# Performance work log

Measured on AMD Instinct MI355X. Metric: run time of the kernel, lower is better.

Reference implementation:

```python
import jax, jax.numpy as jnp
import numpy as np


def _rot_mat(thetas, scales):
    # thetas, scales: [bs, g] -> [bs, g, 9, 9] bilinear-interpolation matrices
    bs, g = thetas.shape
    t = thetas.reshape(-1)
    s = scales.reshape(-1)
    x = jnp.cos(t) * s
    y = jnp.sin(t) * s
    yp = -y
    z = jnp.zeros_like(x)
    o = jnp.ones_like(x)
    a = x - y; b = x * y; c = x + y; d = a * c; e = a + c
    ap = x - yp; bp = x * yp; cp = x + yp; dp = ap * cp; ep = ap + cp

    def M(rows):
        # rows: 9 lists of 9 [N]-arrays -> [9, 9, N]
        return jnp.stack([jnp.stack(r, axis=0) for r in rows], axis=0)

    ctr = [z, z, z, z, o, z, z, z, z]

    pb1 = M([
        [a, 1 - a, z, z, z, z, z, z, z],
        [z, 1 - y, y, z, z, z, z, z, z],
        [z, z, a, z, z, 1 - a, z, z, z],
        [y, z, z, 1 - y, z, z, z, z, z],
        ctr,
        [z, z, z, z, z, 1 - y, z, z, y],
        [z, z, z, 1 - a, z, z, a, z, z],
        [z, z, z, z, z, z, y, 1 - y, z],
        [z, z, z, z, z, z, z, 1 - a, a]])
    pb2 = M([
        [a, 1 - a, z, z, z, z, z, z, z],
        [z, x - b, b, z, 1 - c + b, y - b, z, z, z],
        [z, z, a, z, z, 1 - a, z, z, z],
        [b, y - b, z, x - b, 1 - c + b, z, z, z, z],
        ctr,
        [z, z, z, z, 1 - c + b, x - b, z, y - b, b],
        [z, z, z, 1 - a, z, z, a, z, z],
        [z, z, z, y - b, 1 - c + b, z, b, x - b, z],
        [z, z, z, z, z, z, z, 1 - a, a]])
    ps1 = M([
        [d, a - d, z, c - d, 1 - e + d, z, z, z, z],
        [z, x - b, b, z, 1 - c + b, y - b, z, z, z],
        [z, c - d, d, z, 1 - e + d, a - d, z, z, z],
        [b, y - b, z, x - b, 1 - c + b, z, z, z, z],
        ctr,
        [z, z, z, z, 1 - c + b, x - b, z, y - b, b],
        [z, z, z, a - d, 1 - e + d, z, d, c - d, z],
        [z, z, z, y - b, 1 - c + b, z, b, x - b, z],
        [z, z, z, z, 1 - e + d, c - d, z, a - d, d]])
    ps2 = pb2  # identical in the source
    nb1 = M([
        [cp, z, z, 1 - cp, z, z, z, z, z],
        [yp, 1 - yp, z, z, z, z, z, z, z],
        [z, 1 - cp, cp, z, z, z, z, z, z],
        [z, z, z, 1 - yp, z, z, yp, z, z],
        ctr,
        [z, z, yp, z, z, 1 - yp, z, z, z],
        [z, z, z, z, z, z, cp, 1 - cp, z],
        [z, z, z, z, z, z, z, 1 - yp, yp],
        [z, z, z, z, z, 1 - cp, z, z, cp]])
    nb2 = M([
        [cp, z, z, 1 - cp, z, z, z, z, z],
        [bp, x - bp, z, yp - bp, 1 - cp + bp, z, z, z, z],
        [z, 1 - cp, cp, z, z, z, z, z, z],
        [z, z, z, x - bp, 1 - cp + bp, z, bp, yp - bp, z],
        ctr,
        [z, yp - bp, bp, z, 1 - cp + bp, x - bp, z, z, z],
        [z, z, z, z, z, z, cp, 1 - cp, z],
        [z, z, z, z, 1 - cp + bp, yp - bp, z, x - bp, bp],
        [z, z, z, z, z, 1 - cp, z, z, cp]])
    ns1 = M([
        [dp, cp - dp, z, ap - dp, 1 - ep + dp, z, z, z, z],
        [bp, x - bp, z, yp - bp, 1 - cp + bp, z, z, z, z],
        [z, ap - dp, dp, z, 1 - ep + dp, cp - dp, z, z, z],
        [z, yp - bp, bp, z, 1 - cp + bp, x - bp, z, z, z],
        ctr,
        [z, z, z, x - bp, 1 - cp + bp, z, bp, yp - bp, z],
        [z, z, z, cp - dp, 1 - ep + dp, z, dp, ap - dp, z],
        [z, z, z, z, 1 - cp + bp, yp - bp, z, x - bp, bp],
        [z, z, z, z, 1 - ep + dp, ap - dp, z, cp - dp, dp]])
    ns2 = nb2  # mirrors the positive branch where small_2 == big_2

    m_pos = (t >= 0.0)[None, None, :]
    m_big = (s >= 1.0)[None, None, :]
    m_1 = (jnp.abs(t) <= jnp.pi / 4)[None, None, :]
    pos = jnp.where(m_big, jnp.where(m_1, pb1, pb2), jnp.where(m_1, ps1, ps2))
    neg = jnp.where(m_big, jnp.where(m_1, nb1, nb2), jnp.where(m_1, ns1, ns2))
    rot = jnp.where(m_pos, pos, neg)  # [9, 9, bs*g]
    return jnp.transpose(rot, (2, 0, 1)).reshape(bs, g, 9, 9)


def _forward(x, thetas, scales, lambdas, weight):
    # x: [B, Cin, H, W]; weight: [n, Cout, Cin, 3, 3]; thetas/scales/lambdas: [B, n]
    B, Cin, H, W = x.shape
    n, Cout = weight.shape[0], weight.shape[1]
    rot = _rot_mat(thetas, scales) * lambdas[:, :, None, None]  # [B, n, 9, 9]
    w9 = weight.reshape(n, Cout, Cin, 9)
    # per-sample transformed kernel: sum over kernel_number n and source taps j
    w = jnp.einsum('bnij,nocj->bioc', rot, w9)  # [B, 9, Cout, Cin]
    w = jnp.transpose(w, (0, 2, 3, 1)).reshape(B * Cout, Cin, 3, 3)
    xg = x.reshape(1, B * Cin, H, W)
    out = jax.lax.conv_general_dilated(
        xg, w, window_strides=(1, 1), padding=((1, 1), (1, 1)),
        dimension_numbers=('NCHW', 'OIHW', 'NCHW'), feature_group_count=B)
    return out.reshape(B, Cout, H, W)


def setup_inputs() -> dict:
    key = jax.random.key(0)
    ks = jax.random.split(key, 5)
    B, Cin, Cout, H, W, n = 16, 256, 256, 64, 64, 4
    x = jax.random.normal(ks[0], (B, Cin, H, W), dtype=jnp.float32)
    thetas = jax.random.uniform(ks[1], (B, n), minval=-1.2, maxval=1.2, dtype=jnp.float32)
    scales = jax.random.uniform(ks[2], (B, n), minval=0.5, maxval=1.5, dtype=jnp.float32)
    lambdas = jax.nn.softmax(jax.random.normal(ks[3], (B, n), dtype=jnp.float32), axis=-1)
    weight = jax.random.normal(ks[4], (n, Cout, Cin, 3, 3), dtype=jnp.float32) * 0.05
    return {"x": x, "thetas": thetas, "scales": scales, "lambdas": lambdas, "weight": weight}


def reference(x, thetas, scales, lambdas, weight):
    return _forward(x, thetas, scales, lambdas, weight)
```

## Files before the change

kernel.cpp:

```cpp
#include <hip/hip_runtime.h>
#include <cstdint>
#include <cstddef>

typedef unsigned short ushort_t;
typedef __attribute__((ext_vector_type(4))) float f32x4;
typedef __attribute__((ext_vector_type(8))) short s16x8;

#define PI_4F 0.78539816339744830962f

__device__ inline ushort_t f2bf(float f) {
  unsigned int u = __float_as_uint(f);
  u = u + 0x7fffu + ((u >> 16) & 1u);
  return (ushort_t)(u >> 16);
}

__global__ void rot_kernel(const float* __restrict__ thetas, const float* __restrict__ scales,
                           const float* __restrict__ lambdas, float* __restrict__ rot) {
  int tid = threadIdx.x;
  float t = thetas[tid], s = scales[tid], lam = lambdas[tid];
  float xv = cosf(t) * s, yv = sinf(t) * s;
  bool pos = (t >= 0.0f), big = (s >= 1.0f), m1 = (fabsf(t) <= PI_4F);
  float M[81];
#pragma unroll
  for (int i = 0; i < 81; ++i) M[i] = 0.0f;
  M[36 + 4] = 1.0f;
  if (pos) {
    float a = xv - yv, bb = xv * yv, c = xv + yv;
    if (m1 && big) {
      M[0] = a; M[1] = 1 - a;
      M[9 + 1] = 1 - yv; M[9 + 2] = yv;
      M[18 + 2] = a; M[18 + 5] = 1 - a;
      M[27 + 0] = yv; M[27 + 3] = 1 - yv;
      M[45 + 5] = 1 - yv; M[45 + 8] = yv;
      M[54 + 3] = 1 - a; M[54 + 6] = a;
      M[63 + 6] = yv; M[63 + 7] = 1 - yv;
      M[72 + 7] = 1 - a; M[72 + 8] = a;
    } else if (m1) {
      float d = a * c, e = a + c;
      M[0] = d; M[1] = a - d; M[3] = c - d; M[4] = 1 - e + d;
      M[9 + 1] = xv - bb; M[9 + 2] = bb; M[9 + 4] = 1 - c + bb; M[9 + 5] = yv - bb;
      M[18 + 1] = c - d; M[18 + 2] = d; M[18 + 4] = 1 - e + d; M[18 + 5] = a - d;
      M[27 + 0] = bb; M[27 + 1] = yv - bb; M[27 + 3] = xv - bb; M[27 + 4] = 1 - c + bb;
      M[45 + 4] = 1 - c + bb; M[45 + 5] = xv - bb; M[45 + 7] = yv - bb; M[45 + 8] = bb;
      M[54 + 3] = a - d; M[54 + 4] = 1 - e + d; M[54 + 6] = d; M[54 + 7] = c - d;
      M[63 + 3] = yv - bb; M[63 + 4] = 1 - c + bb; M[63 + 6] = bb; M[63 + 7] = xv - bb;
      M[72 + 4] = 1 - e + d; M[72 + 5] = c - d; M[72 + 7] = a - d; M[72 + 8] = d;
    } else {
      M[0] = a; M[1] = 1 - a;
      M[9 + 1] = xv - bb; M[9 + 2] = bb; M[9 + 4] = 1 - c + bb; M[9 + 5] = yv - bb;
      M[18 + 2] = a; M[18 + 5] = 1 - a;
      M[27 + 0] = bb; M[27 + 1] = yv - bb; M[27 + 3] = xv - bb; M[27 + 4] = 1 - c + bb;
      M[45 + 4] = 1 - c + bb; M[45 + 5] = xv - bb; M[45 + 7] = yv - bb; M[45 + 8] = bb;
      M[54 + 3] = 1 - a; M[54 + 6] = a;
      M[63 + 3] = yv - bb; M[63 + 4] = 1 - c + bb; M[63 + 6] = bb; M[63 + 7] = xv - bb;
      M[72 + 7] = 1 - a; M[72 + 8] = a;
    }
  } else {
    float yp = -yv;
    float ap = xv - yp, bp = xv * yp, cp = xv + yp;
    if (m1 && big) {
      M[0] = cp; M[3] = 1 - cp;
      M[9 + 0] = yp; M[9 + 1] = 1 - yp;
      M[18 + 1] = 1 - cp; M[18 + 2] = cp;
      M[27 + 3] = 1 - yp; M[27 + 6] = yp;
      M[45 + 2] = yp; M[45 + 5] = 1 - yp;
      M[54 + 6] = cp; M[54 + 7] = 1 - cp;
      M[63 + 7] = 1 - yp; M[63 + 8] = yp;
      M[72 + 5] = 1 - cp; M[72 + 8] = cp;
    } else if (m1) {
      float dp = ap * cp, ep = ap + cp;
      M[0] = dp; M[1] = cp - dp; M[3] = ap - dp; M[4] = 1 - ep + dp;
      M[9 + 0] = bp; M[9 + 1] = xv - bp; M[9 + 3] = yp - bp; M[9 + 4] = 1 - cp + bp;
      M[18 + 1] = ap - dp; M[18 + 2] = dp; M[18 + 4] = 1 - ep + dp; M[18 + 5] = cp - dp;
      M[27 + 1] = yp - bp; M[27 + 2] = bp; M[27 + 4] = 1 - cp + bp; M[27 + 5] = xv - bp;
      M[45 + 3] = xv - bp; M[45 + 4] = 1 - cp + bp; M[45 + 6] = bp; M[45 + 7] = yp - bp;
      M[54 + 3] = cp - dp; M[54 + 4] = 1 - ep + dp; M[54 + 6] = dp; M[54 + 7] = ap - dp;
      M[63 + 4] = 1 - cp + bp; M[63 + 5] = yp - bp; M[63 + 7] = xv - bp; M[63 + 8] = bp;
      M[72 + 4] = 1 - ep + dp; M[72 + 5] = ap - dp; M[72 + 7] = cp - dp; M[72 + 8] = dp;
    } else {
      M[0] = cp; M[3] = 1 - cp;
      M[9 + 0] = bp; M[9 + 1] = xv - bp; M[9 + 3] = yp - bp; M[9 + 4] = 1 - cp + bp;
      M[18 + 1] = 1 - cp; M[18 + 2] = cp;
      M[27 + 3] = xv - bp; M[27 + 4] = 1 - cp + bp; M[27 + 6] = bp; M[27 + 7] = yp - bp;
      M[45 + 1] = yp - bp; M[45 + 2] = bp; M[45 + 4] = 1 - cp + bp; M[45 + 5] = xv - bp;
      M[54 + 6] = cp; M[54 + 7] = 1 - cp;
      M[63 + 4] = 1 - cp + bp; M[63 + 5] = yp - bp; M[63 + 7] = xv - bp; M[63 + 8] = bp;
      M[72 + 5] = 1 - cp; M[72 + 8] = cp;
    }
  }
  float* r = rot + tid * 81;
#pragma unroll
  for (int i = 0; i < 81; ++i) r[i] = M[i] * lam;
}

__global__ __launch_bounds__(128) void wt_kernel(const float* __restrict__ weight,
                                                 const float* __restrict__ rot,
                                                 ushort_t* __restrict__ wtout) {
  const int o = blockIdx.x, bg = blockIdx.y;
  const int cid = threadIdx.x;
  const int c = cid * 2;
  float wv0[4][9], wv1[4][9];
#pragma unroll
  for (int n = 0; n < 4; ++n) {
    const float* wp = weight + (((size_t)(n * 256 + o)) * 256 + c) * 9;
#pragma unroll
    for (int j = 0; j < 9; ++j) { wv0[n][j] = wp[j]; wv1[n][j] = wp[9 + j]; }
  }
#pragma unroll
  for (int bl = 0; bl < 4; ++bl) {
    const int b = bg * 4 + bl;
#pragma unroll
    for (int i = 0; i < 9; ++i) {
      float a0 = 0.0f, a1 = 0.0f;
#pragma unroll
      for (int n = 0; n < 4; ++n) {
        const float* r = rot + (b * 4 + n) * 81 + i * 9;
#pragma unroll
        for (int j = 0; j < 9; ++j) {
          a0 = fmaf(r[j], wv0[n][j], a0);
          a1 = fmaf(r[j], wv1[n][j], a1);
        }
      }
      unsigned int word = (unsigned int)f2bf(a0) | ((unsigned int)f2bf(a1) << 16);
      *(unsigned int*)&wtout[((size_t)((b * 9 + i) * 256 + o)) * 256 + c] = word;
    }
  }
}

__global__ __launch_bounds__(256) void transpose_kernel(const float* __restrict__ x,
                                                        ushort_t* __restrict__ xpad) {
  __shared__ ushort_t tile[64][68];
  const int b = blockIdx.z, ct = blockIdx.y, st = blockIdx.x;
  const int t = threadIdx.x;
  const int c0 = ct * 64;
  const float* xb = x + ((size_t)(b * 256 + c0)) * 4096 + st * 64;
#pragma unroll
  for (int k = 0; k < 4; ++k) {
    int idx = t + 256 * k;
    int c_l = idx >> 4, w4 = (idx & 15) * 4;
    float4 v = *(const float4*)&xb[(size_t)c_l * 4096 + w4];
    tile[w4 + 0][c_l] = f2bf(v.x);
    tile[w4 + 1][c_l] = f2bf(v.y);
    tile[w4 + 2][c_l] = f2bf(v.z);
    tile[w4 + 3][c_l] = f2bf(v.w);
  }
  __syncthreads();
  const int c4 = (t & 15) * 4, wl = t >> 4;
  const size_t rowbase = (size_t)(b * 4356 + (st + 1) * 66) * 256 + c0;
#pragma unroll
  for (int k = 0; k < 4; ++k) {
    int w = wl + 16 * k;
    uint2 v = *(const uint2*)&tile[w][c4];
    *(uint2*)&xpad[rowbase + (size_t)(w + 1) * 256 + c4] = v;
  }
  if (t < 32) {
    int w = (t & 16) ? 65 : 0;
    int cc = (t & 15) * 4;
    *(uint2*)&xpad[rowbase + (size_t)w * 256 + cc] = make_uint2(0u, 0u);
  }
  if (st == 0 || st == 63) {
    const int h = (st == 0) ? 0 : 65;
    const size_t hb = (size_t)(b * 4356 + h * 66) * 256 + c0;
    for (int idx = t; idx < 66 * 16; idx += 256) {
      int w = idx >> 4, cc = (idx & 15) * 4;
      *(uint2*)&xpad[hb + (size_t)w * 256 + cc] = make_uint2(0u, 0u);
    }
  }
}

__device__ inline void gload16(const ushort_t* g, ushort_t* l) {
  __builtin_amdgcn_global_load_lds(
      (const __attribute__((address_space(1))) unsigned int*)g,
      (__attribute__((address_space(3))) unsigned int*)l, 16, 0, 0);
}

#define WAITB(N)                                                      \
  asm volatile("s_waitcnt vmcnt(" #N ") lgkmcnt(0)\n\ts_barrier" ::: "memory")

__global__ __launch_bounds__(512, 4) void conv_kernel(
    const ushort_t* __restrict__ xpad, const ushort_t* __restrict__ wt,
    float* __restrict__ out) {
  __shared__ __align__(16) ushort_t As0[8192], As1[8192], As2[8192];
  __shared__ __align__(16) ushort_t Bs0[4096], Bs1[4096], Bs2[4096];

  const int id = blockIdx.x;
  const int xcd = id & 7;
  const int jj = id >> 3;
  const int b = xcd * 2 + (jj >> 5);
  const int ntile = jj & 31;

  const int t = threadIdx.x;
  const int wave = t >> 6, lane = t & 63;
  const int wm = wave & 3, wn = wave >> 2;
  const int lr = lane & 15, lq = lane >> 4;
  const int h0 = ntile * 2;

  const ushort_t* wt_b = wt + (size_t)b * 589824;
  const ushort_t* xp_b = xpad + (size_t)b * 1115136;

  const int lrow = t >> 2;
  const int cg8 = (((t & 3) ^ ((t >> 3) & 3)) * 8);
  const int rsw = (lr >> 1) & 3;
  const int aoff = (wm * 64 + lr) * 32 + ((lq ^ rsw) * 8);
  const int boff = (wn * 64 + lr) * 32 + ((lq ^ rsw) * 8);
  const int nrow2 = 2 * (lrow >> 6);

  f32x4 acc[4][4];
#pragma unroll
  for (int i = 0; i < 4; ++i)
#pragma unroll
    for (int j2 = 0; j2 < 4; ++j2) acc[i][j2] = (f32x4)(0.0f);

  auto stage = [&](int ks, ushort_t* Ad, ushort_t* Bd) {
    const int tap = ks >> 3;
    const int c0k = (ks & 7) << 5;
    const int kh = tap / 3, kw = tap - kh * 3;
    const ushort_t* ga = wt_b + ((size_t)(tap * 256 + lrow)) * 256 + c0k + cg8;
    gload16(ga, Ad + wave * 512);
    gload16(ga + 128 * 256, Ad + 4096 + wave * 512);
    const int sp = (h0 + kh) * 66 + kw + lrow + nrow2;
    gload16(xp_b + (size_t)sp * 256 + c0k + cg8, Bd + wave * 512);
  };

  auto compute = [&](const ushort_t* Ab, const ushort_t* Bb) {
    s16x8 bfr[4];
#pragma unroll
    for (int ni = 0; ni < 4; ++ni)
      bfr[ni] = *(const s16x8*)(Bb + boff + ni * 512);
    __builtin_amdgcn_s_setprio(1);
#pragma unroll
    for (int mi = 0; mi < 4; ++mi) {
      s16x8 af = *(const s16x8*)(Ab + aoff + mi * 512);
#pragma unroll
      for (int ni = 0; ni < 4; ++ni)
        acc[mi][ni] = __builtin_amdgcn_mfma_f32_16x16x32_bf16(af, bfr[ni], acc[mi][ni], 0, 0, 0);
    }
    __builtin_amdgcn_s_setprio(0);
  };

  stage(0, As0, Bs0);
  stage(1, As1, Bs1);

#pragma unroll 1
  for (int kk = 0; kk < 23; ++kk) {
    const int ks = kk * 3;
    WAITB(3);
    stage(ks + 2, As2, Bs2);
    compute(As0, Bs0);
    WAITB(3);
    stage(ks + 3, As0, Bs0);
    compute(As1, Bs1);
    WAITB(3);
    stage(ks + 4, As1, Bs1);
    compute(As2, Bs2);
  }
  WAITB(3);
  stage(71, As2, Bs2);
  compute(As0, Bs0);
  WAITB(3);
  compute(As1, Bs1);
  WAITB(0);
  compute(As2, Bs2);

  float* ob = out + ((size_t)(b * 256 + wm * 64)) * 4096 + ntile * 128 + wn * 64 + lr;
#pragma unroll
  for (int mi = 0; mi < 4; ++mi)
#pragma unroll
    for (int r = 0; r < 4; ++r) {
      float* orow = ob + (size_t)(mi * 16 + lq * 4 + r) * 4096;
#pragma unroll
      for (int ni = 0; ni < 4; ++ni) orow[ni * 16] = acc[mi][ni][r];
    }
}

extern "C" void kernel_launch(void* const* d_in, const int* in_sizes, int n_in,
                              void* d_out, int out_size, void* d_ws, size_t ws_size,
                              hipStream_t stream) {
  const float* x = (const float*)d_in[0];
  const float* thetas = (const float*)d_in[1];
  const float* scales = (const float*)d_in[2];
  const float* lambdas = (const float*)d_in[3];
  const float* weight = (const float*)d_in[4];
  float* out = (float*)d_out;

  float* rot_ws = (float*)d_ws;
  ushort_t* wt_ws = (ushort_t*)((char*)d_ws + 32768);
  ushort_t* xpad_ws = (ushort_t*)((char*)d_ws + 32768 + 18874368);

  rot_kernel<<<1, 64, 0, stream>>>(thetas, scales, lambdas, rot_ws);
  wt_kernel<<<dim3(256, 4), 128, 0, stream>>>(weight, rot_ws, wt_ws);
  transpose_kernel<<<dim3(64, 4, 16), 256, 0, stream>>>(x, xpad_ws);
  conv_kernel<<<512, 512, 0, stream>>>(xpad_ws, wt_ws, out);
}
```

Measured before the change: 235.2 us.

## Fuse rotation matrix build into weight kernel; halve conv waves with larger per-wave tiles

The separate rot_kernel launch is removed: each wt_kernel block now computes its 16 rotation matrices into shared memory, which saves a launch and a global round trip at the cost of some redundant trig work across blocks. The conv kernel drops from 8 waves to 4 waves per block. Each wave now covers 128 output channels (8x4 MFMA tiles instead of 4x4), so each thread issues more async loads per stage and the wait counts change to match. The s_setprio hints are removed. This raises register pressure per wave in exchange for more reuse of the B fragments and less LDS read traffic per MFMA.

```diff
diff --git a/kernel.cpp b/kernel.cpp
--- a/kernel.cpp
+++ b/kernel.cpp
@@ -14,13 +14,9 @@
   return (ushort_t)(u >> 16);
 }
 
-__global__ void rot_kernel(const float* __restrict__ thetas, const float* __restrict__ scales,
-                           const float* __restrict__ lambdas, float* __restrict__ rot) {
-  int tid = threadIdx.x;
-  float t = thetas[tid], s = scales[tid], lam = lambdas[tid];
+__device__ void rot_compute(float t, float s, float* M) {
   float xv = cosf(t) * s, yv = sinf(t) * s;
   bool pos = (t >= 0.0f), big = (s >= 1.0f), m1 = (fabsf(t) <= PI_4F);
-  float M[81];
 #pragma unroll
   for (int i = 0; i < 81; ++i) M[i] = 0.0f;
   M[36 + 4] = 1.0f;
@@ -88,17 +84,17 @@
       M[72 + 5] = 1 - cp; M[72 + 8] = cp;
     }
   }
-  float* r = rot + tid * 81;
-#pragma unroll
-  for (int i = 0; i < 81; ++i) r[i] = M[i] * lam;
 }
 
 __global__ __launch_bounds__(128) void wt_kernel(const float* __restrict__ weight,
-                                                 const float* __restrict__ rot,
+                                                 const float* __restrict__ thetas,
+                                                 const float* __restrict__ scales,
+                                                 const float* __restrict__ lambdas,
                                                  ushort_t* __restrict__ wtout) {
+  __shared__ float rotl[16][81];
   const int o = blockIdx.x, bg = blockIdx.y;
-  const int cid = threadIdx.x;
-  const int c = cid * 2;
+  const int tloc = threadIdx.x;
+  const int c = tloc * 2;
   float wv0[4][9], wv1[4][9];
 #pragma unroll
   for (int n = 0; n < 4; ++n) {
@@ -106,6 +102,15 @@
 #pragma unroll
     for (int j = 0; j < 9; ++j) { wv0[n][j] = wp[j]; wv1[n][j] = wp[9 + j]; }
   }
+  if (tloc < 16) {
+    int gid = bg * 16 + tloc;
+    float M[81];
+    rot_compute(thetas[gid], scales[gid], M);
+    float lam = lambdas[gid];
+#pragma unroll
+    for (int i = 0; i < 81; ++i) rotl[tloc][i] = M[i] * lam;
+  }
+  __syncthreads();
 #pragma unroll
   for (int bl = 0; bl < 4; ++bl) {
     const int b = bg * 4 + bl;
@@ -114,7 +119,7 @@
       float a0 = 0.0f, a1 = 0.0f;
 #pragma unroll
       for (int n = 0; n < 4; ++n) {
-        const float* r = rot + (b * 4 + n) * 81 + i * 9;
+        const float* r = &rotl[bl * 4 + n][i * 9];
 #pragma unroll
         for (int j = 0; j < 9; ++j) {
           a0 = fmaf(r[j], wv0[n][j], a0);
@@ -177,7 +182,7 @@
 #define WAITB(N)                                                      \
   asm volatile("s_waitcnt vmcnt(" #N ") lgkmcnt(0)\n\ts_barrier" ::: "memory")
 
-__global__ __launch_bounds__(512, 4) void conv_kernel(
+__global__ __launch_bounds__(256, 2) void conv_kernel(
     const ushort_t* __restrict__ xpad, const ushort_t* __restrict__ wt,
     float* __restrict__ out) {
   __shared__ __align__(16) ushort_t As0[8192], As1[8192], As2[8192];
@@ -191,7 +196,7 @@
 
   const int t = threadIdx.x;
   const int wave = t >> 6, lane = t & 63;
-  const int wm = wave & 3, wn = wave >> 2;
+  const int wm = wave & 1, wn = wave >> 1;
   const int lr = lane & 15, lq = lane >> 4;
   const int h0 = ntile * 2;
 
@@ -201,13 +206,12 @@
   const int lrow = t >> 2;
   const int cg8 = (((t & 3) ^ ((t >> 3) & 3)) * 8);
   const int rsw = (lr >> 1) & 3;
-  const int aoff = (wm * 64 + lr) * 32 + ((lq ^ rsw) * 8);
+  const int aoff = (wm * 128 + lr) * 32 + ((lq ^ rsw) * 8);
   const int boff = (wn * 64 + lr) * 32 + ((lq ^ rsw) * 8);
-  const int nrow2 = 2 * (lrow >> 6);
-
-  f32x4 acc[4][4];
-#pragma unroll
-  for (int i = 0; i < 4; ++i)
+
+  f32x4 acc[8][4];
+#pragma unroll
+  for (int i = 0; i < 8; ++i)
 #pragma unroll
     for (int j2 = 0; j2 < 4; ++j2) acc[i][j2] = (f32x4)(0.0f);
 
@@ -217,9 +221,12 @@
     const int kh = tap / 3, kw = tap - kh * 3;
     const ushort_t* ga = wt_b + ((size_t)(tap * 256 + lrow)) * 256 + c0k + cg8;
     gload16(ga, Ad + wave * 512);
+    gload16(ga + 64 * 256, Ad + 2048 + wave * 512);
     gload16(ga + 128 * 256, Ad + 4096 + wave * 512);
-    const int sp = (h0 + kh) * 66 + kw + lrow + nrow2;
+    gload16(ga + 192 * 256, Ad + 6144 + wave * 512);
+    const int sp = (h0 + kh) * 66 + kw + lrow;
     gload16(xp_b + (size_t)sp * 256 + c0k + cg8, Bd + wave * 512);
+    gload16(xp_b + (size_t)(sp + 66) * 256 + c0k + cg8, Bd + 2048 + wave * 512);
   };
 
   auto compute = [&](const ushort_t* Ab, const ushort_t* Bb) {
@@ -227,15 +234,13 @@
 #pragma unroll
     for (int ni = 0; ni < 4; ++ni)
       bfr[ni] = *(const s16x8*)(Bb + boff + ni * 512);
-    __builtin_amdgcn_s_setprio(1);
-#pragma unroll
-    for (int mi = 0; mi < 4; ++mi) {
+#pragma unroll
+    for (int mi = 0; mi < 8; ++mi) {
       s16x8 af = *(const s16x8*)(Ab + aoff + mi * 512);
 #pragma unroll
       for (int ni = 0; ni < 4; ++ni)
         acc[mi][ni] = __builtin_amdgcn_mfma_f32_16x16x32_bf16(af, bfr[ni], acc[mi][ni], 0, 0, 0);
     }
-    __builtin_amdgcn_s_setprio(0);
   };
 
   stage(0, As0, Bs0);
@@ -244,27 +249,27 @@
 #pragma unroll 1
   for (int kk = 0; kk < 23; ++kk) {
     const int ks = kk * 3;
-    WAITB(3);
+    WAITB(6);
     stage(ks + 2, As2, Bs2);
     compute(As0, Bs0);
-    WAITB(3);
+    WAITB(6);
     stage(ks + 3, As0, Bs0);
     compute(As1, Bs1);
-    WAITB(3);
+    WAITB(6);
     stage(ks + 4, As1, Bs1);
     compute(As2, Bs2);
   }
-  WAITB(3);
+  WAITB(6);
   stage(71, As2, Bs2);
   compute(As0, Bs0);
-  WAITB(3);
+  WAITB(6);
   compute(As1, Bs1);
   WAITB(0);
   compute(As2, Bs2);
 
-  float* ob = out + ((size_t)(b * 256 + wm * 64)) * 4096 + ntile * 128 + wn * 64 + lr;
-#pragma unroll
-  for (int mi = 0; mi < 4; ++mi)
+  float* ob = out + ((size_t)(b * 256 + wm * 128)) * 4096 + ntile * 128 + wn * 64 + lr;
+#pragma unroll
+  for (int mi = 0; mi < 8; ++mi)
 #pragma unroll
     for (int r = 0; r < 4; ++r) {
       float* orow = ob + (size_t)(mi * 16 + lq * 4 + r) * 4096;
@@ -283,12 +288,10 @@
   const float* weight = (const float*)d_in[4];
   float* out = (float*)d_out;
 
-  float* rot_ws = (float*)d_ws;
-  ushort_t* wt_ws = (ushort_t*)((char*)d_ws + 32768);
-  ushort_t* xpad_ws = (ushort_t*)((char*)d_ws + 32768 + 18874368);
-
-  rot_kernel<<<1, 64, 0, stream>>>(thetas, scales, lambdas, rot_ws);
-  wt_kernel<<<dim3(256, 4), 128, 0, stream>>>(weight, rot_ws, wt_ws);
+  ushort_t* wt_ws = (ushort_t*)d_ws;
+  ushort_t* xpad_ws = (ushort_t*)((char*)d_ws + 18874368);
+
+  wt_kernel<<<dim3(256, 4), 128, 0, stream>>>(weight, thetas, scales, lambdas, wt_ws);
   transpose_kernel<<<dim3(64, 4, 16), 256, 0, stream>>>(x, xpad_ws);
-  conv_kernel<<<512, 512, 0, stream>>>(xpad_ws, wt_ws, out);
-}
+  conv_kernel<<<512, 256, 0, stream>>>(xpad_ws, wt_ws, out);
+}
```

After: 215.8 us. 8.2% less time.
